# Kernel optimization log

Hardware: AMD Instinct MI355X
Metric: run time of the kernel (lower is better)

The kernel has to match this reference:

```python
import jax, jax.numpy as jnp
import numpy as np

B, T, F_IN, H, L = 32, 2000, 80, 512, 2


def _ln(x, g, b, eps=1e-5):
    m = x.mean(-1, keepdims=True)
    v = x.var(-1, keepdims=True)
    return (x - m) / jnp.sqrt(v + eps) * g + b


def setup_inputs() -> dict:
    key = jax.random.key(0)
    ks = jax.random.split(key, 6)
    s = lambda k, shape, sc: jax.random.normal(k, shape, jnp.float32) * sc
    return {
        "x": s(ks[0], (B, T, F_IN), 1.0),
        "W_proj": s(ks[1], (F_IN, H), (1.0 / F_IN) ** 0.5),
        "b_proj": jnp.zeros((H,), jnp.float32),
        "ln1_g": jnp.ones((H,), jnp.float32),
        "ln1_b": jnp.zeros((H,), jnp.float32),
        "W_in": s(ks[2], (L, H, H), (1.0 / H) ** 0.5),
        "W_rec": s(ks[3], (L, H, H), (1.0 / H) ** 0.5),
        "b_rnn": jnp.zeros((L, H), jnp.float32),
        "tau_raw": jnp.ones((L, H), jnp.float32),
        "lno_g": jnp.ones((H,), jnp.float32),
        "lno_b": jnp.zeros((H,), jnp.float32),
    }


def _ltc_layer(x_tbh, W_i, W_r, b, tau_raw):
    # Liquid Time-Constant cell: tau*dh/dt = -h + tanh(Wx + Uh + b), dt = 1
    tau = jax.nn.softplus(tau_raw) + 0.1  # per-unit time constant, >0
    xz = jnp.einsum('tbf,fh->tbh', x_tbh, W_i) + b  # precompute input drive

    def step(h, xz_t):
        z = xz_t + h @ W_r
        h_new = h + (-h + jnp.tanh(z)) / tau
        return h_new, h_new

    h0 = jnp.zeros((x_tbh.shape[1], W_r.shape[0]), x_tbh.dtype)
    h_last, ys = jax.lax.scan(step, h0, xz)
    return ys, h_last


def reference(x, W_proj, b_proj, ln1_g, ln1_b, W_in, W_rec, b_rnn, tau_raw, lno_g, lno_b):
    # input projection: Linear -> LayerNorm -> GELU (dropout=0 in eval)
    h = jax.nn.gelu(_ln(x @ W_proj + b_proj, ln1_g, ln1_b), approximate=False)
    seq = jnp.transpose(h, (1, 0, 2))  # [T, B, H] for scan
    finals = []
    for l in range(W_in.shape[0]):
        seq, h_last = _ltc_layer(seq, W_in[l], W_rec[l], b_rnn[l], tau_raw[l])
        finals.append(h_last)
    encoded = _ln(jnp.transpose(seq, (1, 0, 2)), lno_g, lno_b)  # [B, T, H]
    hidden = jnp.stack(finals)  # [L, B, H]
    return encoded, hidden
```

## Files before the change

kernel.cpp:

```cpp
#include <hip/hip_runtime.h>
#include <math.h>

#define B_    32
#define T_    2000
#define FIN_  80
#define H_    512
#define ROWS_ (B_ * T_)
#define BTH_  ((size_t)ROWS_ * H_)
#define BH_   (B_ * H_)

typedef unsigned long long u64;
typedef unsigned int u32;

__global__ __launch_bounds__(256) void proj_ln_gelu(
    const float* __restrict__ x, const float* __restrict__ Wp,
    const float* __restrict__ bp, const float* __restrict__ g1,
    const float* __restrict__ be1, float* __restrict__ out)
{
  __shared__ float xs[16][84];
  __shared__ float pr[16][512];
  __shared__ float mv[16][2];
  const int tid = threadIdx.x;
  const int r0 = blockIdx.x * 16;

  for (int f = tid; f < 320; f += 256) {
    int rr = f / 20, c4 = (f % 20) * 4;
    int r = r0 + rr; int b = r & 31; int t = r >> 5;
    float4 v = *(const float4*)(x + ((size_t)(b * T_ + t)) * FIN_ + c4);
    xs[rr][c4+0] = v.x; xs[rr][c4+1] = v.y; xs[rr][c4+2] = v.z; xs[rr][c4+3] = v.w;
  }
  __syncthreads();

  const int j = tid;
  float acc0[16], acc1[16];
#pragma unroll
  for (int rr = 0; rr < 16; ++rr) { acc0[rr] = 0.f; acc1[rr] = 0.f; }

  for (int k4 = 0; k4 < 20; ++k4) {
    float w0[4], w1[4];
#pragma unroll
    for (int i = 0; i < 4; ++i) {
      w0[i] = Wp[(k4*4+i)*H_ + j];
      w1[i] = Wp[(k4*4+i)*H_ + j + 256];
    }
#pragma unroll
    for (int rr = 0; rr < 16; ++rr) {
      float4 xv = *(const float4*)&xs[rr][k4*4];
      acc0[rr] += xv.x*w0[0] + xv.y*w0[1] + xv.z*w0[2] + xv.w*w0[3];
      acc1[rr] += xv.x*w1[0] + xv.y*w1[1] + xv.z*w1[2] + xv.w*w1[3];
    }
  }

  const float bj0 = bp[j], bj1 = bp[j+256];
#pragma unroll
  for (int rr = 0; rr < 16; ++rr) {
    pr[rr][j]     = acc0[rr] + bj0;
    pr[rr][j+256] = acc1[rr] + bj1;
  }
  __syncthreads();

  const int wv = tid >> 6, ln = tid & 63;
  for (int rr = wv*4; rr < wv*4+4; ++rr) {
    float s = 0.f, ss = 0.f;
#pragma unroll
    for (int q = 0; q < 8; ++q) { float v = pr[rr][ln + q*64]; s += v; ss += v*v; }
#pragma unroll
    for (int o = 32; o > 0; o >>= 1) { s += __shfl_xor(s, o, 64); ss += __shfl_xor(ss, o, 64); }
    if (ln == 0) {
      float m = s * (1.f/512.f);
      float var = ss * (1.f/512.f) - m*m;
      mv[rr][0] = m; mv[rr][1] = 1.f / sqrtf(var + 1e-5f);
    }
  }
  __syncthreads();

  const float ga0 = g1[j], ga1 = g1[j+256], bo0 = be1[j], bo1 = be1[j+256];
#pragma unroll
  for (int rr = 0; rr < 16; ++rr) {
    float m = mv[rr][0], rs = mv[rr][1];
    float v0 = (pr[rr][j]     - m) * rs * ga0 + bo0;
    float v1 = (pr[rr][j+256] - m) * rs * ga1 + bo1;
    v0 = v0 * 0.5f * (1.f + erff(v0 * 0.70710678118654752f));
    v1 = v1 * 0.5f * (1.f + erff(v1 * 0.70710678118654752f));
    size_t ro = (size_t)(r0 + rr) * H_;
    out[ro + j] = v0; out[ro + j + 256] = v1;
  }
}

__global__ __launch_bounds__(256) void gemm512(
    const float* __restrict__ A, const float* __restrict__ Bm,
    const float* __restrict__ bias, float* __restrict__ C)
{
  __shared__ float As[16][132];
  __shared__ float Bs[16][132];
  const int tid = threadIdx.x;
  const int n0 = blockIdx.x * 128;
  const int m0 = blockIdx.y * 128;
  const int tx = tid & 15, ty = tid >> 4;

  float acc[8][8];
#pragma unroll
  for (int i = 0; i < 8; ++i)
#pragma unroll
    for (int jj = 0; jj < 8; ++jj) acc[i][jj] = 0.f;

  float4 pa[2], pb[2];
#pragma unroll
  for (int i = 0; i < 2; ++i) {
    int f = i*256 + tid;
    int mm = f >> 2, kk4 = (f & 3) * 4;
    pa[i] = *(const float4*)(A + (size_t)(m0+mm)*H_ + kk4);
    int kk = f >> 5, nn4 = (f & 31) * 4;
    pb[i] = *(const float4*)(Bm + (size_t)kk*H_ + n0 + nn4);
  }

  for (int kt = 0; kt < 32; ++kt) {
    __syncthreads();
#pragma unroll
    for (int i = 0; i < 2; ++i) {
      int f = i*256 + tid;
      int mm = f >> 2, kk4 = (f & 3) * 4;
      As[kk4+0][mm] = pa[i].x; As[kk4+1][mm] = pa[i].y;
      As[kk4+2][mm] = pa[i].z; As[kk4+3][mm] = pa[i].w;
      int kk = f >> 5, nn4 = (f & 31) * 4;
      *(float4*)&Bs[kk][nn4] = pb[i];
    }
    __syncthreads();
    if (kt < 31) {
#pragma unroll
      for (int i = 0; i < 2; ++i) {
        int f = i*256 + tid;
        int mm = f >> 2, kk4 = (f & 3) * 4;
        pa[i] = *(const float4*)(A + (size_t)(m0+mm)*H_ + (kt+1)*16 + kk4);
        int kk = f >> 5, nn4 = (f & 31) * 4;
        pb[i] = *(const float4*)(Bm + (size_t)((kt+1)*16+kk)*H_ + n0 + nn4);
      }
    }
#pragma unroll
    for (int k = 0; k < 16; ++k) {
      float a[8], bb[8];
      *(float4*)(a+0) = *(const float4*)&As[k][ty*4];
      *(float4*)(a+4) = *(const float4*)&As[k][ty*4 + 64];
      *(float4*)(bb+0) = *(const float4*)&Bs[k][tx*4];
      *(float4*)(bb+4) = *(const float4*)&Bs[k][tx*4 + 64];
#pragma unroll
      for (int i = 0; i < 8; ++i)
#pragma unroll
        for (int jj = 0; jj < 8; ++jj) acc[i][jj] += a[i] * bb[jj];
    }
  }

  float4 bi0 = *(const float4*)(bias + n0 + tx*4);
  float4 bi1 = *(const float4*)(bias + n0 + tx*4 + 64);
#pragma unroll
  for (int i = 0; i < 8; ++i) {
    int m = m0 + ty*4 + (i & 3) + (i >> 2) * 64;
    float4 v0 = make_float4(acc[i][0]+bi0.x, acc[i][1]+bi0.y, acc[i][2]+bi0.z, acc[i][3]+bi0.w);
    float4 v1 = make_float4(acc[i][4]+bi1.x, acc[i][5]+bi1.y, acc[i][6]+bi1.z, acc[i][7]+bi1.w);
    *(float4*)(C + (size_t)m*H_ + n0 + tx*4)      = v0;
    *(float4*)(C + (size_t)m*H_ + n0 + tx*4 + 64) = v1;
  }
}

__global__ __launch_bounds__(512) void fused_scan(
    const float* __restrict__ Wrc0,
    const float* __restrict__ Win1,
    const float* __restrict__ Wrc1,
    const float* __restrict__ tra,
    const float* __restrict__ brn1,
    const float* __restrict__ lng, const float* __restrict__ lnb,
    float* __restrict__ bufA,
    u64* __restrict__ h0tag,
    u64* __restrict__ h1tag,
    u32* __restrict__ ysflag,
    float* __restrict__ enc,
    float* __restrict__ hid0,
    float* __restrict__ hid1)
{
  __shared__ float hl[1024];
  __shared__ float pt[2048];
  const int tid = threadIdx.x;

  if (blockIdx.x < 256) {
    const int b  = blockIdx.x & 31;
    const int s  = blockIdx.x >> 5;
    const int j0 = s * 64;
    const int kg = tid >> 4;
    const int cq = tid & 15;

    float wreg[64];
    {
      const float* wsrc = Wrc0 + (size_t)(kg * 16) * H_ + j0 + cq * 4;
#pragma unroll
      for (int kk = 0; kk < 16; ++kk) {
        float4 wv = *(const float4*)(wsrc + (size_t)kk * H_);
        wreg[kk*4+0] = wv.x; wreg[kk*4+1] = wv.y; wreg[kk*4+2] = wv.z; wreg[kk*4+3] = wv.w;
      }
    }
    float tau0 = 1.f, tau1 = 1.f;
    if (tid < 32) {
      float tr0 = tra[j0 + 2*tid], tr1 = tra[j0 + 2*tid + 1];
      tau0 = (tr0 > 20.f ? tr0 : log1pf(expf(tr0))) + 0.1f;
      tau1 = (tr1 > 20.f ? tr1 : log1pf(expf(tr1))) + 0.1f;
    }
    __syncthreads();

    for (int t = 0; t < T_; ++t) {
      float2 xzv = make_float2(0.f, 0.f);
      if (tid < 32)
        xzv = *(const float2*)(bufA + ((size_t)t * B_ + b) * H_ + j0 + 2*tid);

      if (t > 0) {
        const u64* rb = h0tag + ((size_t)((t + 1) & 1) * B_ + b) * H_;
        u64 v = __hip_atomic_load(rb + tid, __ATOMIC_RELAXED, __HIP_MEMORY_SCOPE_AGENT);
        while ((u32)(v >> 32) != (u32)t) {
          __builtin_amdgcn_s_sleep(1);
          v = __hip_atomic_load(rb + tid, __ATOMIC_RELAXED, __HIP_MEMORY_SCOPE_AGENT);
        }
        hl[tid] = __uint_as_float((u32)v);
      } else {
        hl[tid] = 0.f;
      }
      __syncthreads();

      float hr[16];
#pragma unroll
      for (int q = 0; q < 4; ++q)
        *(float4*)(hr + q*4) = *(const float4*)(hl + kg*16 + q*4);
      float a0 = 0.f, a1 = 0.f, a2 = 0.f, a3 = 0.f;
#pragma unroll
      for (int kk = 0; kk < 16; ++kk) {
        float h = hr[kk];
        a0 += h * wreg[kk*4+0]; a1 += h * wreg[kk*4+1];
        a2 += h * wreg[kk*4+2]; a3 += h * wreg[kk*4+3];
      }
      *(float4*)&pt[kg*64 + cq*4] = make_float4(a0, a1, a2, a3);
      __syncthreads();

      if (tid < 64) {
        int c2 = tid & 31;
        float s0 = 0.f, s1 = 0.f;
        for (int g = tid >> 5; g < 32; g += 2) {
          float2 p = *(const float2*)&pt[g*64 + c2*2];
          s0 += p.x; s1 += p.y;
        }
        s0 += __shfl_xor(s0, 32, 64);
        s1 += __shfl_xor(s1, 32, 64);
        if (tid < 32) {
          float z0 = xzv.x + s0, z1 = xzv.y + s1;
          float th0 = tanhf(z0), th1 = tanhf(z1);
          float h0v = hl[j0 + 2*tid], h1v = hl[j0 + 2*tid + 1];
          float hn0 = h0v + (th0 - h0v) / tau0;
          float hn1 = h1v + (th1 - h1v) / tau1;
          u64* wb = h0tag + ((size_t)(t & 1) * B_ + b) * H_ + j0 + 2*tid;
          u64 tg = ((u64)(u32)(t + 1)) << 32;
          __hip_atomic_store(wb,     tg | __float_as_uint(hn0), __ATOMIC_RELAXED, __HIP_MEMORY_SCOPE_AGENT);
          __hip_atomic_store(wb + 1, tg | __float_as_uint(hn1), __ATOMIC_RELAXED, __HIP_MEMORY_SCOPE_AGENT);
          union { u64 u; float f[2]; } cv; cv.f[0] = hn0; cv.f[1] = hn1;
          u64* yw = (u64*)bufA + (((size_t)t * B_ + b) * H_ + j0) / 2 + tid;
          __hip_atomic_store(yw, cv.u, __ATOMIC_RELAXED, __HIP_MEMORY_SCOPE_AGENT);
          if (t == T_ - 1)
            *(float2*)(hid0 + b*H_ + j0 + 2*tid) = make_float2(hn0, hn1);
        }
      }
      if (tid == 0) {
        asm volatile("s_waitcnt vmcnt(0)" ::: "memory");
        __hip_atomic_fetch_or(ysflag + (size_t)t * B_ + b, 1u << s,
                              __ATOMIC_RELAXED, __HIP_MEMORY_SCOPE_AGENT);
      }
      __syncthreads();
    }
  } else {
    const int idx = blockIdx.x - 256;
    const int b  = idx >> 4;
    const int s  = idx & 15;
    const int j0 = s * 32;
    const int kg = tid >> 3;
    const int cq = tid & 7;

    float wreg[64];
    {
      const float* wsrc = (kg < 32)
          ? (Win1 + (size_t)(kg * 16) * H_ + j0 + cq * 4)
          : (Wrc1 + (size_t)((kg - 32) * 16) * H_ + j0 + cq * 4);
#pragma unroll
      for (int kk = 0; kk < 16; ++kk) {
        float4 wv = *(const float4*)(wsrc + (size_t)kk * H_);
        wreg[kk*4+0] = wv.x; wreg[kk*4+1] = wv.y; wreg[kk*4+2] = wv.z; wreg[kk*4+3] = wv.w;
      }
    }
    float tauc = 1.f, bic = 0.f, gc = 1.f, bcc = 0.f;
    if (tid < 32) {
      float tr = tra[H_ + j0 + tid];
      tauc = (tr > 20.f ? tr : log1pf(expf(tr))) + 0.1f;
      bic = brn1[j0 + tid];
      gc = lng[j0 + tid];
      bcc = lnb[j0 + tid];
    }
    __syncthreads();

    for (int t = 0; t < T_; ++t) {
      if (tid == 0) {
        while (__hip_atomic_load(ysflag + (size_t)t * B_ + b,
                                 __ATOMIC_RELAXED, __HIP_MEMORY_SCOPE_AGENT) != 0xFFu)
          __builtin_amdgcn_s_sleep(1);
      }
      __syncthreads();

      const u64* rb = h1tag + ((size_t)((t + 1) & 1) * B_ + b) * H_;
      u64 hv = 0;
      if (t > 0)
        hv = __hip_atomic_load(rb + tid, __ATOMIC_RELAXED, __HIP_MEMORY_SCOPE_AGENT);
      if (tid < 256) {
        u64 yv = __hip_atomic_load((const u64*)bufA + ((size_t)t * B_ + b) * (H_/2) + tid,
                                   __ATOMIC_RELAXED, __HIP_MEMORY_SCOPE_AGENT);
        union { u64 u; float f[2]; } cv; cv.u = yv;
        hl[2*tid]     = cv.f[0];
        hl[2*tid + 1] = cv.f[1];
      }
      if (t > 0) {
        while ((u32)(hv >> 32) != (u32)t) {
          __builtin_amdgcn_s_sleep(1);
          hv = __hip_atomic_load(rb + tid, __ATOMIC_RELAXED, __HIP_MEMORY_SCOPE_AGENT);
        }
        hl[512 + tid] = __uint_as_float((u32)hv);
      } else {
        hl[512 + tid] = 0.f;
      }
      __syncthreads();

      float hr[16];
#pragma unroll
      for (int q = 0; q < 4; ++q)
        *(float4*)(hr + q*4) = *(const float4*)(hl + kg*16 + q*4);
      float a0 = 0.f, a1 = 0.f, a2 = 0.f, a3 = 0.f;
#pragma unroll
      for (int kk = 0; kk < 16; ++kk) {
        float h = hr[kk];
        a0 += h * wreg[kk*4+0]; a1 += h * wreg[kk*4+1];
        a2 += h * wreg[kk*4+2]; a3 += h * wreg[kk*4+3];
      }
      *(float4*)&pt[kg*32 + cq*4] = make_float4(a0, a1, a2, a3);
      __syncthreads();

      if (tid < 64) {
        int c = tid & 31;
        float ps = 0.f;
        for (int g = tid >> 5; g < 64; g += 2) ps += pt[g*32 + c];
        ps += __shfl_xor(ps, 32, 64);
        float hn = 0.f, hold = 0.f;
        if (tid < 32) {
          float z = ps + bic;
          float th = tanhf(z);
          hold = hl[512 + j0 + tid];
          hn = hold + (th - hold) / tauc;
          u64* wb = h1tag + ((size_t)(t & 1) * B_ + b) * H_ + j0 + tid;
          __hip_atomic_store(wb, (((u64)(u32)(t + 1)) << 32) | __float_as_uint(hn),
                             __ATOMIC_RELAXED, __HIP_MEMORY_SCOPE_AGENT);
          if (t == T_ - 1) hid1[b*H_ + j0 + tid] = hn;
        }
        if (t > 0) {
          float sm = 0.f, ss = 0.f;
#pragma unroll
          for (int q = 0; q < 8; ++q) {
            float v = hl[512 + tid*8 + q];
            sm += v; ss += v*v;
          }
#pragma unroll
          for (int o = 32; o > 0; o >>= 1) {
            sm += __shfl_xor(sm, o, 64);
            ss += __shfl_xor(ss, o, 64);
          }
          float m = sm * (1.f/512.f);
          float rs = 1.f / sqrtf(ss * (1.f/512.f) - m*m + 1e-5f);
          if (tid < 32)
            enc[((size_t)b * T_ + (t - 1)) * H_ + j0 + tid] = (hold - m) * rs * gc + bcc;
        }
      }
      __syncthreads();
    }

    {
      const u64* rb = h1tag + ((size_t)((T_ - 1) & 1) * B_ + b) * H_;
      u64 v = __hip_atomic_load(rb + tid, __ATOMIC_RELAXED, __HIP_MEMORY_SCOPE_AGENT);
      while ((u32)(v >> 32) != (u32)T_) {
        __builtin_amdgcn_s_sleep(1);
        v = __hip_atomic_load(rb + tid, __ATOMIC_RELAXED, __HIP_MEMORY_SCOPE_AGENT);
      }
      hl[512 + tid] = __uint_as_float((u32)v);
      __syncthreads();
      if (tid < 64) {
        float sm = 0.f, ss = 0.f;
#pragma unroll
        for (int q = 0; q < 8; ++q) {
          float vv = hl[512 + tid*8 + q];
          sm += vv; ss += vv*vv;
        }
#pragma unroll
        for (int o = 32; o > 0; o >>= 1) {
          sm += __shfl_xor(sm, o, 64);
          ss += __shfl_xor(ss, o, 64);
        }
        float m = sm * (1.f/512.f);
        float rs = 1.f / sqrtf(ss * (1.f/512.f) - m*m + 1e-5f);
        if (tid < 32) {
          float hold = hl[512 + j0 + tid];
          enc[((size_t)b * T_ + (T_ - 1)) * H_ + j0 + tid] = (hold - m) * rs * gc + bcc;
        }
      }
    }
  }
}

extern "C" void kernel_launch(void* const* d_in, const int* in_sizes, int n_in,
                              void* d_out, int out_size, void* d_ws, size_t ws_size,
                              hipStream_t stream)
{
  (void)in_sizes; (void)n_in; (void)out_size;
  const float* x   = (const float*)d_in[0];
  const float* Wp  = (const float*)d_in[1];
  const float* bp  = (const float*)d_in[2];
  const float* g1  = (const float*)d_in[3];
  const float* be1 = (const float*)d_in[4];
  const float* Win = (const float*)d_in[5];
  const float* Wrc = (const float*)d_in[6];
  const float* brn = (const float*)d_in[7];
  const float* tra = (const float*)d_in[8];
  const float* gno = (const float*)d_in[9];
  const float* bno = (const float*)d_in[10];
  float* outp = (float*)d_out;

  const size_t H0T_BYTES = (size_t)2 * B_ * H_ * 8;
  const size_t SYNC_BYTES = 786432;
  const size_t BUFA_BYTES = BTH_ * 4;

  char* sync;
  float* bufA;
  if (ws_size >= SYNC_BYTES + BUFA_BYTES) {
    sync = (char*)d_ws;
    bufA = (float*)((char*)d_ws + SYNC_BYTES);
  } else {
    sync = (char*)d_in[0];
    bufA = (float*)d_ws;
  }
  u64* h0tag  = (u64*)sync;
  u64* h1tag  = (u64*)(sync + H0T_BYTES);
  u32* ysflag = (u32*)(sync + 2 * H0T_BYTES);

  proj_ln_gelu<<<dim3(ROWS_/16), 256, 0, stream>>>(x, Wp, bp, g1, be1, outp);

  gemm512<<<dim3(4, ROWS_/128), 256, 0, stream>>>(outp, Win, brn, bufA);

  hipMemsetAsync(sync, 0, SYNC_BYTES, stream);

  fused_scan<<<768, 512, 0, stream>>>(
      Wrc, Win + H_*H_, Wrc + H_*H_, tra, brn + H_, gno, bno,
      bufA, h0tag, h1tag, ysflag,
      outp, outp + BTH_, outp + BTH_ + BH_);
}
```

Baseline: 9.998 ms.

## Process two batch rows per layer-1 scan block to halve block count

Layer-1 blocks in the fused persistent scan now each handle two batch elements, reusing the register-resident weight slice for both, which halves the grid from 768 to 512 blocks. Shared buffers double and launch bounds request two blocks per CU so that all persistent blocks stay co-resident. The aim is fewer blocks competing for CUs and better amortisation of weight registers and barriers. The cost is a longer per-step critical path in layer-1 blocks and more register and LDS pressure.

```diff
diff --git a/kernel.cpp b/kernel.cpp
--- a/kernel.cpp
+++ b/kernel.cpp
@@ -162,7 +162,7 @@
   }
 }
 
-__global__ __launch_bounds__(512) void fused_scan(
+__global__ __launch_bounds__(512, 2) void fused_scan(
     const float* __restrict__ Wrc0,
     const float* __restrict__ Win1,
     const float* __restrict__ Wrc1,
@@ -177,8 +177,8 @@
     float* __restrict__ hid0,
     float* __restrict__ hid1)
 {
-  __shared__ float hl[1024];
-  __shared__ float pt[2048];
+  __shared__ float hl[2048];
+  __shared__ float pt[4096];
   const int tid = threadIdx.x;
 
   if (blockIdx.x < 256) {
@@ -272,11 +272,12 @@
     }
   } else {
     const int idx = blockIdx.x - 256;
-    const int b  = idx >> 4;
+    const int p  = idx >> 4;
     const int s  = idx & 15;
     const int j0 = s * 32;
     const int kg = tid >> 3;
     const int cq = tid & 7;
+    const int b0 = 2 * p;
 
     float wreg[64];
     {
@@ -290,80 +291,95 @@
       }
     }
     float tauc = 1.f, bic = 0.f, gc = 1.f, bcc = 0.f;
-    if (tid < 32) {
-      float tr = tra[H_ + j0 + tid];
+    if (tid < 128) {
+      int c = tid & 31;
+      float tr = tra[H_ + j0 + c];
       tauc = (tr > 20.f ? tr : log1pf(expf(tr))) + 0.1f;
-      bic = brn1[j0 + tid];
-      gc = lng[j0 + tid];
-      bcc = lnb[j0 + tid];
+      bic = brn1[j0 + c];
+      gc = lng[j0 + c];
+      bcc = lnb[j0 + c];
     }
     __syncthreads();
 
     for (int t = 0; t < T_; ++t) {
-      if (tid == 0) {
-        while (__hip_atomic_load(ysflag + (size_t)t * B_ + b,
+      if (tid < 2) {
+        while (__hip_atomic_load(ysflag + (size_t)t * B_ + b0 + tid,
                                  __ATOMIC_RELAXED, __HIP_MEMORY_SCOPE_AGENT) != 0xFFu)
           __builtin_amdgcn_s_sleep(1);
       }
       __syncthreads();
 
-      const u64* rb = h1tag + ((size_t)((t + 1) & 1) * B_ + b) * H_;
-      u64 hv = 0;
-      if (t > 0)
-        hv = __hip_atomic_load(rb + tid, __ATOMIC_RELAXED, __HIP_MEMORY_SCOPE_AGENT);
-      if (tid < 256) {
-        u64 yv = __hip_atomic_load((const u64*)bufA + ((size_t)t * B_ + b) * (H_/2) + tid,
+      const u64* rb = h1tag + (size_t)((t + 1) & 1) * B_ * H_;
+      u64 hv0 = 0, hv1 = 0;
+      if (t > 0) {
+        hv0 = __hip_atomic_load(rb + (size_t)b0 * H_ + tid, __ATOMIC_RELAXED, __HIP_MEMORY_SCOPE_AGENT);
+        hv1 = __hip_atomic_load(rb + (size_t)(b0 + 1) * H_ + tid, __ATOMIC_RELAXED, __HIP_MEMORY_SCOPE_AGENT);
+      }
+      {
+        int ub = tid >> 8, off = tid & 255;
+        u64 yv = __hip_atomic_load((const u64*)bufA + ((size_t)t * B_ + b0 + ub) * (H_/2) + off,
                                    __ATOMIC_RELAXED, __HIP_MEMORY_SCOPE_AGENT);
         union { u64 u; float f[2]; } cv; cv.u = yv;
-        hl[2*tid]     = cv.f[0];
-        hl[2*tid + 1] = cv.f[1];
+        hl[ub*1024 + off*2]     = cv.f[0];
+        hl[ub*1024 + off*2 + 1] = cv.f[1];
       }
       if (t > 0) {
-        while ((u32)(hv >> 32) != (u32)t) {
+        while ((u32)(hv0 >> 32) != (u32)t) {
           __builtin_amdgcn_s_sleep(1);
-          hv = __hip_atomic_load(rb + tid, __ATOMIC_RELAXED, __HIP_MEMORY_SCOPE_AGENT);
-        }
-        hl[512 + tid] = __uint_as_float((u32)hv);
+          hv0 = __hip_atomic_load(rb + (size_t)b0 * H_ + tid, __ATOMIC_RELAXED, __HIP_MEMORY_SCOPE_AGENT);
+        }
+        while ((u32)(hv1 >> 32) != (u32)t) {
+          __builtin_amdgcn_s_sleep(1);
+          hv1 = __hip_atomic_load(rb + (size_t)(b0 + 1) * H_ + tid, __ATOMIC_RELAXED, __HIP_MEMORY_SCOPE_AGENT);
+        }
+        hl[512 + tid]  = __uint_as_float((u32)hv0);
+        hl[1536 + tid] = __uint_as_float((u32)hv1);
       } else {
-        hl[512 + tid] = 0.f;
-      }
-      __syncthreads();
-
-      float hr[16];
-#pragma unroll
-      for (int q = 0; q < 4; ++q)
-        *(float4*)(hr + q*4) = *(const float4*)(hl + kg*16 + q*4);
-      float a0 = 0.f, a1 = 0.f, a2 = 0.f, a3 = 0.f;
-#pragma unroll
-      for (int kk = 0; kk < 16; ++kk) {
-        float h = hr[kk];
-        a0 += h * wreg[kk*4+0]; a1 += h * wreg[kk*4+1];
-        a2 += h * wreg[kk*4+2]; a3 += h * wreg[kk*4+3];
-      }
-      *(float4*)&pt[kg*32 + cq*4] = make_float4(a0, a1, a2, a3);
-      __syncthreads();
-
-      if (tid < 64) {
-        int c = tid & 31;
+        hl[512 + tid]  = 0.f;
+        hl[1536 + tid] = 0.f;
+      }
+      __syncthreads();
+
+#pragma unroll
+      for (int u = 0; u < 2; ++u) {
+        float hr[16];
+#pragma unroll
+        for (int q = 0; q < 4; ++q)
+          *(float4*)(hr + q*4) = *(const float4*)(hl + u*1024 + kg*16 + q*4);
+        float a0 = 0.f, a1 = 0.f, a2 = 0.f, a3 = 0.f;
+#pragma unroll
+        for (int kk = 0; kk < 16; ++kk) {
+          float h = hr[kk];
+          a0 += h * wreg[kk*4+0]; a1 += h * wreg[kk*4+1];
+          a2 += h * wreg[kk*4+2]; a3 += h * wreg[kk*4+3];
+        }
+        *(float4*)&pt[u*2048 + kg*32 + cq*4] = make_float4(a0, a1, a2, a3);
+      }
+      __syncthreads();
+
+      if (tid < 128) {
+        const int u = tid >> 6;
+        const int l = tid & 63;
+        const int c = l & 31;
         float ps = 0.f;
-        for (int g = tid >> 5; g < 64; g += 2) ps += pt[g*32 + c];
+        for (int g = l >> 5; g < 64; g += 2) ps += pt[u*2048 + g*32 + c];
         ps += __shfl_xor(ps, 32, 64);
         float hn = 0.f, hold = 0.f;
-        if (tid < 32) {
+        if (l < 32) {
           float z = ps + bic;
           float th = tanhf(z);
-          hold = hl[512 + j0 + tid];
+          hold = hl[u*1024 + 512 + j0 + l];
           hn = hold + (th - hold) / tauc;
-          u64* wb = h1tag + ((size_t)(t & 1) * B_ + b) * H_ + j0 + tid;
+          u64* wb = h1tag + ((size_t)(t & 1) * B_ + b0 + u) * H_ + j0 + l;
           __hip_atomic_store(wb, (((u64)(u32)(t + 1)) << 32) | __float_as_uint(hn),
                              __ATOMIC_RELAXED, __HIP_MEMORY_SCOPE_AGENT);
-          if (t == T_ - 1) hid1[b*H_ + j0 + tid] = hn;
+          if (t == T_ - 1) hid1[(b0 + u)*H_ + j0 + l] = hn;
         }
         if (t > 0) {
           float sm = 0.f, ss = 0.f;
 #pragma unroll
           for (int q = 0; q < 8; ++q) {
-            float v = hl[512 + tid*8 + q];
+            float v = hl[u*1024 + 512 + l*8 + q];
             sm += v; ss += v*v;
           }
 #pragma unroll
@@ -373,27 +389,35 @@
           }
           float m = sm * (1.f/512.f);
           float rs = 1.f / sqrtf(ss * (1.f/512.f) - m*m + 1e-5f);
-          if (tid < 32)
-            enc[((size_t)b * T_ + (t - 1)) * H_ + j0 + tid] = (hold - m) * rs * gc + bcc;
+          if (l < 32)
+            enc[((size_t)(b0 + u) * T_ + (t - 1)) * H_ + j0 + l] = (hold - m) * rs * gc + bcc;
         }
       }
       __syncthreads();
     }
 
     {
-      const u64* rb = h1tag + ((size_t)((T_ - 1) & 1) * B_ + b) * H_;
-      u64 v = __hip_atomic_load(rb + tid, __ATOMIC_RELAXED, __HIP_MEMORY_SCOPE_AGENT);
-      while ((u32)(v >> 32) != (u32)T_) {
+      const u64* rb = h1tag + (size_t)((T_ - 1) & 1) * B_ * H_;
+      u64 v0 = __hip_atomic_load(rb + (size_t)b0 * H_ + tid, __ATOMIC_RELAXED, __HIP_MEMORY_SCOPE_AGENT);
+      while ((u32)(v0 >> 32) != (u32)T_) {
         __builtin_amdgcn_s_sleep(1);
-        v = __hip_atomic_load(rb + tid, __ATOMIC_RELAXED, __HIP_MEMORY_SCOPE_AGENT);
-      }
-      hl[512 + tid] = __uint_as_float((u32)v);
-      __syncthreads();
-      if (tid < 64) {
+        v0 = __hip_atomic_load(rb + (size_t)b0 * H_ + tid, __ATOMIC_RELAXED, __HIP_MEMORY_SCOPE_AGENT);
+      }
+      u64 v1 = __hip_atomic_load(rb + (size_t)(b0 + 1) * H_ + tid, __ATOMIC_RELAXED, __HIP_MEMORY_SCOPE_AGENT);
+      while ((u32)(v1 >> 32) != (u32)T_) {
+        __builtin_amdgcn_s_sleep(1);
+        v1 = __hip_atomic_load(rb + (size_t)(b0 + 1) * H_ + tid, __ATOMIC_RELAXED, __HIP_MEMORY_SCOPE_AGENT);
+      }
+      hl[512 + tid]  = __uint_as_float((u32)v0);
+      hl[1536 + tid] = __uint_as_float((u32)v1);
+      __syncthreads();
+      if (tid < 128) {
+        const int u = tid >> 6;
+        const int l = tid & 63;
         float sm = 0.f, ss = 0.f;
 #pragma unroll
         for (int q = 0; q < 8; ++q) {
-          float vv = hl[512 + tid*8 + q];
+          float vv = hl[u*1024 + 512 + l*8 + q];
           sm += vv; ss += vv*vv;
         }
 #pragma unroll
@@ -403,9 +427,9 @@
         }
         float m = sm * (1.f/512.f);
         float rs = 1.f / sqrtf(ss * (1.f/512.f) - m*m + 1e-5f);
-        if (tid < 32) {
-          float hold = hl[512 + j0 + tid];
-          enc[((size_t)b * T_ + (T_ - 1)) * H_ + j0 + tid] = (hold - m) * rs * gc + bcc;
+        if (l < 32) {
+          float hold = hl[u*1024 + 512 + j0 + l];
+          enc[((size_t)(b0 + u) * T_ + (T_ - 1)) * H_ + j0 + l] = (hold - m) * rs * gc + bcc;
         }
       }
     }
@@ -453,7 +477,7 @@
 
   hipMemsetAsync(sync, 0, SYNC_BYTES, stream);
 
-  fused_scan<<<768, 512, 0, stream>>>(
+  fused_scan<<<512, 512, 0, stream>>>(
       Wrc, Win + H_*H_, Wrc + H_*H_, tra, brn + H_, gno, bno,
       bufA, h0tag, h1tag, ysflag,
       outp, outp + BTH_, outp + BTH_ + BH_);
```

Result: slower. 10.83 ms (+8.3%).
